# Optimization experiments

Hardware: AMD Instinct MI355X
Metric: run time of the kernel (lower is better)

Reference implementation:

```python
import jax, jax.numpy as jnp
import numpy as np

T, B, NIN = 256, 256, 512
NH, NEMB = 512, 256


def setup_inputs() -> dict:
    key = jax.random.key(0)
    ks = jax.random.split(key, 11)
    s = 0.02  # small init to keep tanh/sigmoid in active range
    return {
        "feats": jax.random.normal(ks[0], (T, B, NIN), jnp.float32),
        "h": jax.random.normal(ks[1], (B, NH), jnp.float32),
        "cur_embed": jax.random.normal(ks[2], (B, NEMB), jnp.float32),
        # i2h: Linear(nIn, nHidden, bias=False)
        "w_i2h": jax.random.normal(ks[3], (NH, NIN), jnp.float32) * s,
        # h2h: Linear(nHidden, nHidden) with bias
        "w_h2h": jax.random.normal(ks[4], (NH, NH), jnp.float32) * s,
        "b_h2h": jax.random.normal(ks[5], (NH,), jnp.float32) * s,
        # score: Linear(nHidden, 1, bias=False)
        "w_score": jax.random.normal(ks[6], (NH,), jnp.float32) * s,
        # GRUCell(nIn + num_embeddings, nHidden); gate order r, z, n
        "w_ih": jax.random.normal(ks[7], (3 * NH, NIN + NEMB), jnp.float32) * s,
        "w_hh": jax.random.normal(ks[8], (3 * NH, NH), jnp.float32) * s,
        "b_ih": jax.random.normal(ks[9], (3 * NH,), jnp.float32) * s,
        "b_hh": jax.random.normal(ks[10], (3 * NH,), jnp.float32) * s,
    }


def reference(feats, h, cur_embed, w_i2h, w_h2h, b_h2h, w_score,
              w_ih, w_hh, b_ih, b_hh):
    # MORAN branch, test=True (FractionalPickup is skipped at eval time).
    # feats: [T, B, nIn], h: [B, nHidden], cur_embed: [B, nEmb]
    feats_ = jnp.einsum('tbc,hc->tbh', feats, w_i2h)          # i2h, [T,B,H]
    h_ = h @ w_h2h.T + b_h2h                                   # h2h, [B,H]
    emit = jnp.einsum('tbh,h->tb', jnp.tanh(feats_ + h_[None]), w_score)
    alpha = jax.nn.softmax(emit, axis=0)                       # softmax over T
    context = jnp.einsum('tb,tbc->bc', alpha, feats)           # [B,nIn]
    x = jnp.concatenate([context, cur_embed], axis=1)          # [B,nIn+nEmb]
    # GRUCell
    gi = x @ w_ih.T + b_ih                                     # [B,3H]
    gh = h @ w_hh.T + b_hh                                     # [B,3H]
    gi_r, gi_z, gi_n = jnp.split(gi, 3, axis=1)
    gh_r, gh_z, gh_n = jnp.split(gh, 3, axis=1)
    r = jax.nn.sigmoid(gi_r + gh_r)
    z = jax.nn.sigmoid(gi_z + gh_z)
    n = jnp.tanh(gi_n + r * gh_n)
    nh = (1.0 - z) * n + z * h
    return nh, alpha
```

## Files before the change

kernel.cpp:

```cpp
#include <hip/hip_runtime.h>

typedef __bf16 bf16;
typedef __bf16 bf16x4 __attribute__((ext_vector_type(4)));
typedef __bf16 bf16x8 __attribute__((ext_vector_type(8)));
typedef float  f32x4  __attribute__((ext_vector_type(4)));

#define T_DIM 256
#define B_DIM 256
#define NIN   512
#define NH    512
#define NEMB  256
#define NX    768
#define NG    1536

__device__ __forceinline__ float fast_tanh(float x) {
    float e = __expf(2.0f * x);
    return 1.0f - 2.0f * __builtin_amdgcn_rcpf(e + 1.0f);
}
__device__ __forceinline__ float fast_sigmoid(float x) {
    return __builtin_amdgcn_rcpf(1.0f + __expf(-x));
}

__device__ __forceinline__ void gload_lds16(const bf16* g, bf16* l) {
    __builtin_amdgcn_global_load_lds(
        (const __attribute__((address_space(1))) void*)g,
        (__attribute__((address_space(3))) void*)l, 16, 0, 0);
}

__device__ __forceinline__ int swz(int rc) { return ((rc >> 1) & 3) << 3; }

__global__ __launch_bounds__(256) void cvt_weights(
    const float* __restrict__ a0, const float* __restrict__ a1,
    const float* __restrict__ a2, const float* __restrict__ a3,
    const float* __restrict__ a4,
    bf16* __restrict__ b0, bf16* __restrict__ b1, bf16* __restrict__ b2,
    bf16* __restrict__ b3, bf16* __restrict__ b4) {
    const int N0 = 65536, N1 = 131072, N2 = 425984, N3 = 622592, N4 = 655360;
    for (int i = blockIdx.x * 256 + threadIdx.x; i < N4; i += gridDim.x * 256) {
        const float* s; bf16* d; int j; bool img = false;
        if (i < N0)      { s = a0; d = b0; j = i; img = true; }
        else if (i < N1) { s = a1; d = b1; j = i - N0; }
        else if (i < N2) { s = a2; d = b2; j = i - N1; }
        else if (i < N3) { s = a3; d = b3; j = i - N2; }
        else             { s = a4; d = b4; j = i - N3; }
        float4 v = reinterpret_cast<const float4*>(s)[j];
        bf16x4 o = { (bf16)v.x, (bf16)v.y, (bf16)v.z, (bf16)v.w };
        if (img) {
            int e = j * 4, col = e >> 9, kc = e & 511, kk = kc >> 5, k = kc & 31;
            int off = kk * 16384 + col * 32 + (k ^ swz(col));
            *reinterpret_cast<bf16x4*>(d + off) = o;
        } else {
            reinterpret_cast<bf16x4*>(d)[j] = o;
        }
    }
}

__global__ __launch_bounds__(256) void gemm_bias(
    const bf16* __restrict__ A, const bf16* __restrict__ B,
    const float* __restrict__ bias, float* __restrict__ C,
    int M, int N, int K) {
    __shared__ bf16 At[64][40];
    __shared__ bf16 Bt[64][40];
    const int tid = threadIdx.x;
    const int m0 = blockIdx.y * 64, n0 = blockIdx.x * 64;
    const int wid = tid >> 6, lane = tid & 63, hi = lane >> 4, lo = lane & 15;
    const int srow = tid >> 2, sseg = tid & 3;
    f32x4 acc[4] = {};

    for (int kk = 0; kk < K; kk += 32) {
        bf16x8 av = *reinterpret_cast<const bf16x8*>(A + (size_t)(m0 + srow) * K + kk + sseg * 8);
        bf16x8 bv = *reinterpret_cast<const bf16x8*>(B + (size_t)(n0 + srow) * K + kk + sseg * 8);
        __syncthreads();
        *reinterpret_cast<bf16x8*>(&At[srow][sseg * 8]) = av;
        *reinterpret_cast<bf16x8*>(&Bt[srow][sseg * 8]) = bv;
        __syncthreads();
        bf16x8 a = *reinterpret_cast<const bf16x8*>(&At[wid * 16 + lo][hi * 8]);
#pragma unroll
        for (int nt = 0; nt < 4; ++nt) {
            bf16x8 b = *reinterpret_cast<const bf16x8*>(&Bt[nt * 16 + lo][hi * 8]);
            acc[nt] = __builtin_amdgcn_mfma_f32_16x16x32_bf16(a, b, acc[nt], 0, 0, 0);
        }
    }
#pragma unroll
    for (int nt = 0; nt < 4; ++nt) {
        int n = n0 + nt * 16 + lo;
        float bv = bias[n];
#pragma unroll
        for (int r = 0; r < 4; ++r) {
            int m = m0 + wid * 16 + hi * 4 + r;
            C[(size_t)m * N + n] = acc[nt][r] + bv;
        }
    }
}

__global__ __launch_bounds__(512, 4) void emit_kernel(
    const float* __restrict__ feats, const bf16* __restrict__ Wimg,
    const float* __restrict__ hbuf, const float* __restrict__ wscore,
    float* __restrict__ emit_out) {
    __shared__ bf16 Btile[2][16384];
    __shared__ bf16 Atile[2][2048];
    __shared__ float ew[512];
    const int tid = threadIdx.x;
    const int m0 = blockIdx.x * 64;
    const int wid = tid >> 6, lane = tid & 63, hi = lane >> 4, lo = lane & 15;

    const int arow = tid >> 3, akq = tid & 7;
    const int aoff = arow * 32 + ((akq * 4) ^ swz(arow));
    const float* asrc = feats + (size_t)(m0 + arow) * NIN + akq * 4;

#pragma unroll
    for (int r = 0; r < 4; ++r)
        gload_lds16(Wimg + r * 4096 + wid * 512 + lane * 8,
                    &Btile[0][r * 4096 + wid * 512]);
    {
        float4 fa = *reinterpret_cast<const float4*>(asrc);
        bf16x4 o = { (bf16)fa.x, (bf16)fa.y, (bf16)fa.z, (bf16)fa.w };
        *reinterpret_cast<bf16x4*>(&Atile[0][aoff]) = o;
    }
    __syncthreads();

    f32x4 acc[4][4] = {};
    float4 fa;
    for (int kk = 0; kk < 16; ++kk) {
        const int cur = kk & 1, nxt = cur ^ 1;
        if (kk < 15) {
            fa = *reinterpret_cast<const float4*>(asrc + (kk + 1) * 32);
#pragma unroll
            for (int r = 0; r < 4; ++r)
                gload_lds16(Wimg + (kk + 1) * 16384 + r * 4096 + wid * 512 + lane * 8,
                            &Btile[nxt][r * 4096 + wid * 512]);
        }

        bf16x8 a[4], b[4];
#pragma unroll
        for (int st = 0; st < 4; ++st) {
            int row = st * 16 + lo;
            a[st] = *reinterpret_cast<const bf16x8*>(
                &Atile[cur][row * 32 + ((hi * 8) ^ swz(row))]);
        }
#pragma unroll
        for (int nt = 0; nt < 4; ++nt) {
            int col = wid * 64 + nt * 16 + lo;
            b[nt] = *reinterpret_cast<const bf16x8*>(
                &Btile[cur][col * 32 + ((hi * 8) ^ swz(col))]);
        }
#pragma unroll
        for (int nt = 0; nt < 4; ++nt)
#pragma unroll
            for (int st = 0; st < 4; ++st)
                acc[nt][st] = __builtin_amdgcn_mfma_f32_16x16x32_bf16(a[st], b[nt], acc[nt][st], 0, 0, 0);

        if (kk < 15) {
            bf16x4 o = { (bf16)fa.x, (bf16)fa.y, (bf16)fa.z, (bf16)fa.w };
            *reinterpret_cast<bf16x4*>(&Atile[nxt][aoff]) = o;
        }
        __syncthreads();
    }

    float ep[4][4] = {};
    const int bbase = m0 & (B_DIM - 1);
    const int n0 = wid * 64;
#pragma unroll
    for (int nt = 0; nt < 4; ++nt) {
        int n = n0 + nt * 16 + lo;
        float wsn = wscore[n];
#pragma unroll
        for (int st = 0; st < 4; ++st) {
#pragma unroll
            for (int r = 0; r < 4; ++r) {
                int b = bbase + st * 16 + hi * 4 + r;
                float x = acc[nt][st][r] + hbuf[(size_t)b * NH + n];
                ep[st][r] += fast_tanh(x) * wsn;
            }
        }
    }
#pragma unroll
    for (int st = 0; st < 4; ++st)
#pragma unroll
        for (int r = 0; r < 4; ++r)
#pragma unroll
            for (int off = 1; off < 16; off <<= 1)
                ep[st][r] += __shfl_xor(ep[st][r], off, 64);

    if (lo == 0) {
#pragma unroll
        for (int st = 0; st < 4; ++st)
#pragma unroll
            for (int r = 0; r < 4; ++r)
                ew[wid * 64 + st * 16 + hi * 4 + r] = ep[st][r];
    }
    __syncthreads();
    if (tid < 64) {
        float s = 0.0f;
#pragma unroll
        for (int ww = 0; ww < 8; ++ww) s += ew[ww * 64 + tid];
        emit_out[m0 + tid] = s;
    }
}

__global__ __launch_bounds__(256) void softmax_t(
    const float* __restrict__ emit, float* __restrict__ alpha, float* __restrict__ out_alpha) {
    int b = blockIdx.x, t = threadIdx.x;
    int wv = t >> 6, ln = t & 63;
    float e = emit[(size_t)t * B_DIM + b];
    float m = e;
#pragma unroll
    for (int off = 32; off; off >>= 1) m = fmaxf(m, __shfl_xor(m, off, 64));
    __shared__ float red[4], red2[4];
    if (ln == 0) red[wv] = m;
    __syncthreads();
    m = fmaxf(fmaxf(red[0], red[1]), fmaxf(red[2], red[3]));
    float p = __expf(e - m);
    float s = p;
#pragma unroll
    for (int off = 32; off; off >>= 1) s += __shfl_xor(s, off, 64);
    if (ln == 0) red2[wv] = s;
    __syncthreads();
    float inv = __builtin_amdgcn_rcpf(red2[0] + red2[1] + red2[2] + red2[3]);
    float a = p * inv;
    alpha[(size_t)t * B_DIM + b] = a;
    out_alpha[(size_t)t * B_DIM + b] = a;
}

__global__ __launch_bounds__(256) void ctx_kernel(
    const float* __restrict__ feats, const float* __restrict__ alpha,
    const float* __restrict__ emb, bf16* __restrict__ x) {
    int b = blockIdx.x;
    __shared__ float al[T_DIM];
    __shared__ float red[4][512];
    int tid = threadIdx.x;
    al[tid] = alpha[(size_t)tid * B_DIM + b];
    __syncthreads();
    int c8 = tid & 63, tq = tid >> 6;
    float acc[8] = {};
    for (int t = tq * 64; t < tq * 64 + 64; ++t) {
        const float* src = feats + ((size_t)(t * B_DIM + b)) * NIN + c8 * 8;
        float4 v0 = *reinterpret_cast<const float4*>(src);
        float4 v1 = *reinterpret_cast<const float4*>(src + 4);
        float a = al[t];
        acc[0] += a * v0.x; acc[1] += a * v0.y; acc[2] += a * v0.z; acc[3] += a * v0.w;
        acc[4] += a * v1.x; acc[5] += a * v1.y; acc[6] += a * v1.z; acc[7] += a * v1.w;
    }
#pragma unroll
    for (int j = 0; j < 8; ++j) red[tq][c8 * 8 + j] = acc[j];
    __syncthreads();
#pragma unroll
    for (int k = 0; k < 2; ++k) {
        int c = tid * 2 + k;
        float s = red[0][c] + red[1][c] + red[2][c] + red[3][c];
        x[(size_t)b * NX + c] = (bf16)s;
    }
    x[(size_t)b * NX + NIN + tid] = (bf16)emb[(size_t)b * NEMB + tid];
}

__global__ __launch_bounds__(256) void gru_kernel(
    const float* __restrict__ gi, const float* __restrict__ gh,
    const float* __restrict__ h, float* __restrict__ out) {
    int idx = blockIdx.x * 256 + threadIdx.x;
    int b = idx >> 9, j = idx & 511;
    const float* gib = gi + (size_t)b * NG;
    const float* ghb = gh + (size_t)b * NG;
    float r = fast_sigmoid(gib[j] + ghb[j]);
    float z = fast_sigmoid(gib[NH + j] + ghb[NH + j]);
    float n = fast_tanh(gib[2 * NH + j] + r * ghb[2 * NH + j]);
    out[idx] = (1.0f - z) * n + z * h[idx];
}

extern "C" void kernel_launch(void* const* d_in, const int* in_sizes, int n_in,
                              void* d_out, int out_size, void* d_ws, size_t ws_size,
                              hipStream_t stream) {
    const float* feats = (const float*)d_in[0];
    const float* h     = (const float*)d_in[1];
    const float* emb   = (const float*)d_in[2];
    const float* w_i2h = (const float*)d_in[3];
    const float* w_h2h = (const float*)d_in[4];
    const float* b_h2h = (const float*)d_in[5];
    const float* w_sc  = (const float*)d_in[6];
    const float* w_ih  = (const float*)d_in[7];
    const float* w_hh  = (const float*)d_in[8];
    const float* b_ih  = (const float*)d_in[9];
    const float* b_hh  = (const float*)d_in[10];
    float* out = (float*)d_out;

    char* ws = (char*)d_ws;
    bf16*  Wimg    = (bf16*)(ws);
    bf16*  w_h2h_b = (bf16*)(ws + 524288);
    bf16*  w_ih_b  = (bf16*)(ws + 1048576);
    bf16*  w_hh_b  = (bf16*)(ws + 3407872);
    bf16*  h_b     = (bf16*)(ws + 4980736);
    bf16*  x_b     = (bf16*)(ws + 5242880);
    float* hbuf    = (float*)(ws + 5636096);
    float* emit    = (float*)(ws + 6160384);
    float* alpha   = (float*)(ws + 6422528);
    float* gi      = (float*)(ws + 6684672);
    float* gh      = (float*)(ws + 8257536);

    cvt_weights<<<1024, 256, 0, stream>>>(w_i2h, w_h2h, w_ih, w_hh, h,
                                          Wimg, w_h2h_b, w_ih_b, w_hh_b, h_b);

    gemm_bias<<<dim3(8, 4), 256, 0, stream>>>(h_b, w_h2h_b, b_h2h, hbuf, 256, NH, NH);

    emit_kernel<<<1024, 512, 0, stream>>>(feats, Wimg, hbuf, w_sc, emit);

    softmax_t<<<256, 256, 0, stream>>>(emit, alpha, out + 131072);

    ctx_kernel<<<256, 256, 0, stream>>>(feats, alpha, emb, x_b);

    gemm_bias<<<dim3(24, 4), 256, 0, stream>>>(x_b, w_ih_b, b_ih, gi, 256, NG, NX);
    gemm_bias<<<dim3(24, 4), 256, 0, stream>>>(h_b, w_hh_b, b_hh, gh, 256, NG, NH);

    gru_kernel<<<512, 256, 0, stream>>>(gi, gh, h, out);
}
```

Measured before the change: 122.6 us.

## Load attention weight fragments directly into registers with deeper prefetch in emit kernel

The emit GEMM no longer stages the bf16 image-projection weights through a double-buffered LDS tile via global_load_lds. Each lane now reads its B fragments straight from global memory into registers, three stages deep, and feats is prefetched three iterations ahead. The loop is fully unrolled with hand-placed waitcnt and barriers in place of __syncthreads. This cuts about 64KB of LDS and the LDS round trip for B, but raises register pressure, so launch bounds drop from 4 to 2 blocks per CU. It also relies on the pre-swizzled weight layout being readable with per-lane global loads.

```diff
diff --git a/kernel.cpp b/kernel.cpp
--- a/kernel.cpp
+++ b/kernel.cpp
@@ -19,12 +19,6 @@
 }
 __device__ __forceinline__ float fast_sigmoid(float x) {
     return __builtin_amdgcn_rcpf(1.0f + __expf(-x));
-}
-
-__device__ __forceinline__ void gload_lds16(const bf16* g, bf16* l) {
-    __builtin_amdgcn_global_load_lds(
-        (const __attribute__((address_space(1))) void*)g,
-        (__attribute__((address_space(3))) void*)l, 16, 0, 0);
 }
 
 __device__ __forceinline__ int swz(int rc) { return ((rc >> 1) & 3) << 3; }
@@ -93,11 +87,10 @@
     }
 }
 
-__global__ __launch_bounds__(512, 4) void emit_kernel(
+__global__ __launch_bounds__(512, 2) void emit_kernel(
     const float* __restrict__ feats, const bf16* __restrict__ Wimg,
     const float* __restrict__ hbuf, const float* __restrict__ wscore,
     float* __restrict__ emit_out) {
-    __shared__ bf16 Btile[2][16384];
     __shared__ bf16 Atile[2][2048];
     __shared__ float ew[512];
     const int tid = threadIdx.x;
@@ -108,53 +101,61 @@
     const int aoff = arow * 32 + ((akq * 4) ^ swz(arow));
     const float* asrc = feats + (size_t)(m0 + arow) * NIN + akq * 4;
 
-#pragma unroll
-    for (int r = 0; r < 4; ++r)
-        gload_lds16(Wimg + r * 4096 + wid * 512 + lane * 8,
-                    &Btile[0][r * 4096 + wid * 512]);
+    const int col0 = wid * 64 + lo;
+    const bf16* bsrc = Wimg + col0 * 32 + ((hi * 8) ^ swz(col0));
+
+    float4 fa[3];
+    bf16x8 bfr[3][4];
+
+    fa[0] = *reinterpret_cast<const float4*>(asrc);
+    fa[1] = *reinterpret_cast<const float4*>(asrc + 32);
+    fa[2] = *reinterpret_cast<const float4*>(asrc + 64);
+#pragma unroll
+    for (int s = 0; s < 2; ++s)
+#pragma unroll
+        for (int nt = 0; nt < 4; ++nt)
+            bfr[s][nt] = *reinterpret_cast<const bf16x8*>(bsrc + s * 16384 + nt * 512);
     {
-        float4 fa = *reinterpret_cast<const float4*>(asrc);
-        bf16x4 o = { (bf16)fa.x, (bf16)fa.y, (bf16)fa.z, (bf16)fa.w };
+        bf16x4 o = { (bf16)fa[0].x, (bf16)fa[0].y, (bf16)fa[0].z, (bf16)fa[0].w };
         *reinterpret_cast<bf16x4*>(&Atile[0][aoff]) = o;
     }
-    __syncthreads();
+    asm volatile("s_waitcnt lgkmcnt(0)" ::: "memory");
+    __builtin_amdgcn_s_barrier();
+    __builtin_amdgcn_sched_barrier(0);
 
     f32x4 acc[4][4] = {};
-    float4 fa;
+#pragma unroll
     for (int kk = 0; kk < 16; ++kk) {
-        const int cur = kk & 1, nxt = cur ^ 1;
-        if (kk < 15) {
-            fa = *reinterpret_cast<const float4*>(asrc + (kk + 1) * 32);
-#pragma unroll
-            for (int r = 0; r < 4; ++r)
-                gload_lds16(Wimg + (kk + 1) * 16384 + r * 4096 + wid * 512 + lane * 8,
-                            &Btile[nxt][r * 4096 + wid * 512]);
-        }
-
-        bf16x8 a[4], b[4];
+        if (kk + 3 < 16)
+            fa[kk % 3] = *reinterpret_cast<const float4*>(asrc + (kk + 3) * 32);
+        if (kk + 2 < 16) {
+#pragma unroll
+            for (int nt = 0; nt < 4; ++nt)
+                bfr[(kk + 2) % 3][nt] =
+                    *reinterpret_cast<const bf16x8*>(bsrc + (kk + 2) * 16384 + nt * 512);
+        }
+        bf16x8 a[4];
 #pragma unroll
         for (int st = 0; st < 4; ++st) {
             int row = st * 16 + lo;
             a[st] = *reinterpret_cast<const bf16x8*>(
-                &Atile[cur][row * 32 + ((hi * 8) ^ swz(row))]);
-        }
-#pragma unroll
-        for (int nt = 0; nt < 4; ++nt) {
-            int col = wid * 64 + nt * 16 + lo;
-            b[nt] = *reinterpret_cast<const bf16x8*>(
-                &Btile[cur][col * 32 + ((hi * 8) ^ swz(col))]);
+                &Atile[kk & 1][row * 32 + ((hi * 8) ^ swz(row))]);
         }
 #pragma unroll
         for (int nt = 0; nt < 4; ++nt)
 #pragma unroll
             for (int st = 0; st < 4; ++st)
-                acc[nt][st] = __builtin_amdgcn_mfma_f32_16x16x32_bf16(a[st], b[nt], acc[nt][st], 0, 0, 0);
-
-        if (kk < 15) {
-            bf16x4 o = { (bf16)fa.x, (bf16)fa.y, (bf16)fa.z, (bf16)fa.w };
-            *reinterpret_cast<bf16x4*>(&Atile[nxt][aoff]) = o;
-        }
-        __syncthreads();
+                acc[nt][st] = __builtin_amdgcn_mfma_f32_16x16x32_bf16(
+                    a[st], bfr[kk % 3][nt], acc[nt][st], 0, 0, 0);
+        if (kk + 1 < 16) {
+            float4 f = fa[(kk + 1) % 3];
+            bf16x4 o = { (bf16)f.x, (bf16)f.y, (bf16)f.z, (bf16)f.w };
+            *reinterpret_cast<bf16x4*>(&Atile[(kk + 1) & 1][aoff]) = o;
+            asm volatile("s_waitcnt lgkmcnt(0)" ::: "memory");
+            __builtin_amdgcn_sched_barrier(0);
+            __builtin_amdgcn_s_barrier();
+            __builtin_amdgcn_sched_barrier(0);
+        }
     }
 
     float ep[4][4] = {};
```

Result: slower. 128.3 us (+4.7%).

## Triple-buffer emit kernel B tiles with manual waitcnt and single barrier

Applied to the files above, without the earlier changes.

Converts the emit GEMM's weight tile staging from double to triple buffering with prefetch distance two. The per-iteration __syncthreads pair is replaced by explicit vmcnt/lgkmcnt waits and one s_barrier, and the loop is fully unrolled. This hides more global-load latency behind MFMA work, at the cost of more LDS (three 32KB B buffers), which drops the occupancy hint. The reduction scratch now reuses Atile, and the h-to-hidden GRU GEMM launch is moved earlier in the stream with no functional change.

```diff
diff --git a/kernel.cpp b/kernel.cpp
--- a/kernel.cpp
+++ b/kernel.cpp
@@ -93,13 +93,12 @@
     }
 }
 
-__global__ __launch_bounds__(512, 4) void emit_kernel(
+__global__ __launch_bounds__(512) void emit_kernel(
     const float* __restrict__ feats, const bf16* __restrict__ Wimg,
     const float* __restrict__ hbuf, const float* __restrict__ wscore,
     float* __restrict__ emit_out) {
-    __shared__ bf16 Btile[2][16384];
+    __shared__ bf16 Btile[3][16384];
     __shared__ bf16 Atile[2][2048];
-    __shared__ float ew[512];
     const int tid = threadIdx.x;
     const int m0 = blockIdx.x * 64;
     const int wid = tid >> 6, lane = tid & 63, hi = lane >> 4, lo = lane & 15;
@@ -108,27 +107,44 @@
     const int aoff = arow * 32 + ((akq * 4) ^ swz(arow));
     const float* asrc = feats + (size_t)(m0 + arow) * NIN + akq * 4;
 
+    float4 fav0 = *reinterpret_cast<const float4*>(asrc);
+    float4 fav1 = *reinterpret_cast<const float4*>(asrc + 32);
 #pragma unroll
     for (int r = 0; r < 4; ++r)
-        gload_lds16(Wimg + r * 4096 + wid * 512 + lane * 8,
+        gload_lds16(Wimg + 0 * 16384 + r * 4096 + wid * 512 + lane * 8,
                     &Btile[0][r * 4096 + wid * 512]);
+#pragma unroll
+    for (int r = 0; r < 4; ++r)
+        gload_lds16(Wimg + 1 * 16384 + r * 4096 + wid * 512 + lane * 8,
+                    &Btile[1][r * 4096 + wid * 512]);
     {
-        float4 fa = *reinterpret_cast<const float4*>(asrc);
-        bf16x4 o = { (bf16)fa.x, (bf16)fa.y, (bf16)fa.z, (bf16)fa.w };
+        bf16x4 o = { (bf16)fav0.x, (bf16)fav0.y, (bf16)fav0.z, (bf16)fav0.w };
         *reinterpret_cast<bf16x4*>(&Atile[0][aoff]) = o;
     }
-    __syncthreads();
+    asm volatile("s_waitcnt lgkmcnt(0)" ::: "memory");
+    __builtin_amdgcn_sched_barrier(0);
 
     f32x4 acc[4][4] = {};
-    float4 fa;
+
+#pragma unroll
     for (int kk = 0; kk < 16; ++kk) {
-        const int cur = kk & 1, nxt = cur ^ 1;
         if (kk < 15) {
-            fa = *reinterpret_cast<const float4*>(asrc + (kk + 1) * 32);
+            asm volatile("s_waitcnt vmcnt(5)" ::: "memory");
+        } else {
+            asm volatile("s_waitcnt vmcnt(0)" ::: "memory");
+        }
+        __builtin_amdgcn_s_barrier();
+        __builtin_amdgcn_sched_barrier(0);
+
+        if (kk < 14) {
+            if ((kk & 1) == 0)
+                fav0 = *reinterpret_cast<const float4*>(asrc + (kk + 2) * 32);
+            else
+                fav1 = *reinterpret_cast<const float4*>(asrc + (kk + 2) * 32);
 #pragma unroll
             for (int r = 0; r < 4; ++r)
-                gload_lds16(Wimg + (kk + 1) * 16384 + r * 4096 + wid * 512 + lane * 8,
-                            &Btile[nxt][r * 4096 + wid * 512]);
+                gload_lds16(Wimg + (kk + 2) * 16384 + r * 4096 + wid * 512 + lane * 8,
+                            &Btile[(kk + 2) % 3][r * 4096 + wid * 512]);
         }
 
         bf16x8 a[4], b[4];
@@ -136,25 +152,28 @@
         for (int st = 0; st < 4; ++st) {
             int row = st * 16 + lo;
             a[st] = *reinterpret_cast<const bf16x8*>(
-                &Atile[cur][row * 32 + ((hi * 8) ^ swz(row))]);
+                &Atile[kk & 1][row * 32 + ((hi * 8) ^ swz(row))]);
         }
 #pragma unroll
         for (int nt = 0; nt < 4; ++nt) {
             int col = wid * 64 + nt * 16 + lo;
             b[nt] = *reinterpret_cast<const bf16x8*>(
-                &Btile[cur][col * 32 + ((hi * 8) ^ swz(col))]);
+                &Btile[kk % 3][col * 32 + ((hi * 8) ^ swz(col))]);
         }
 #pragma unroll
         for (int nt = 0; nt < 4; ++nt)
 #pragma unroll
             for (int st = 0; st < 4; ++st)
-                acc[nt][st] = __builtin_amdgcn_mfma_f32_16x16x32_bf16(a[st], b[nt], acc[nt][st], 0, 0, 0);
+                acc[nt][st] = __builtin_amdgcn_mfma_f32_16x16x32_bf16(
+                    a[st], b[nt], acc[nt][st], 0, 0, 0);
 
         if (kk < 15) {
-            bf16x4 o = { (bf16)fa.x, (bf16)fa.y, (bf16)fa.z, (bf16)fa.w };
-            *reinterpret_cast<bf16x4*>(&Atile[nxt][aoff]) = o;
-        }
-        __syncthreads();
+            float4 f = ((kk + 1) & 1) ? fav1 : fav0;
+            bf16x4 o = { (bf16)f.x, (bf16)f.y, (bf16)f.z, (bf16)f.w };
+            *reinterpret_cast<bf16x4*>(&Atile[(kk + 1) & 1][aoff]) = o;
+            asm volatile("s_waitcnt lgkmcnt(0)" ::: "memory");
+            __builtin_amdgcn_sched_barrier(0);
+        }
     }
 
     float ep[4][4] = {};
@@ -182,6 +201,8 @@
             for (int off = 1; off < 16; off <<= 1)
                 ep[st][r] += __shfl_xor(ep[st][r], off, 64);
 
+    __syncthreads();
+    float* ew = reinterpret_cast<float*>(&Atile[0][0]);
     if (lo == 0) {
 #pragma unroll
         for (int st = 0; st < 4; ++st)
@@ -299,6 +320,7 @@
                                           Wimg, w_h2h_b, w_ih_b, w_hh_b, h_b);
 
     gemm_bias<<<dim3(8, 4), 256, 0, stream>>>(h_b, w_h2h_b, b_h2h, hbuf, 256, NH, NH);
+    gemm_bias<<<dim3(24, 4), 256, 0, stream>>>(h_b, w_hh_b, b_hh, gh, 256, NG, NH);
 
     emit_kernel<<<1024, 512, 0, stream>>>(feats, Wimg, hbuf, w_sc, emit);
 
@@ -307,7 +329,6 @@
     ctx_kernel<<<256, 256, 0, stream>>>(feats, alpha, emb, x_b);
 
     gemm_bias<<<dim3(24, 4), 256, 0, stream>>>(x_b, w_ih_b, b_ih, gi, 256, NG, NX);
-    gemm_bias<<<dim3(24, 4), 256, 0, stream>>>(h_b, w_hh_b, b_hh, gh, 256, NG, NH);
 
     gru_kernel<<<512, 256, 0, stream>>>(gi, gh, h, out);
 }
```

Result: slower. 141.0 us (+15.0%).

## Enlarge emit GEMM tile to 128 rows with 64-wide K stages

Applied to the files above, without the earlier changes.

The emit kernel now computes 128 rows per block instead of 64, with K stages of 64 and a single LDS buffer. The weight image layout and swizzle are changed to match (8-slot XOR on 16-byte chunks). Each block loads the full weight tile once per stage, so weight traffic per output row is halved and there are fewer barrier rounds. The cost is no double buffering (two syncs per stage), higher register and LDS use (occupancy hint lowered to 2), and half as many blocks. The gh GEMM is also moved earlier and the ctx loop gets an unroll hint.

```diff
diff --git a/kernel.cpp b/kernel.cpp
--- a/kernel.cpp
+++ b/kernel.cpp
@@ -12,6 +12,7 @@
 #define NEMB  256
 #define NX    768
 #define NG    1536
+#define MTOT  65536
 
 __device__ __forceinline__ float fast_tanh(float x) {
     float e = __expf(2.0f * x);
@@ -26,8 +27,6 @@
         (const __attribute__((address_space(1))) void*)g,
         (__attribute__((address_space(3))) void*)l, 16, 0, 0);
 }
-
-__device__ __forceinline__ int swz(int rc) { return ((rc >> 1) & 3) << 3; }
 
 __global__ __launch_bounds__(256) void cvt_weights(
     const float* __restrict__ a0, const float* __restrict__ a1,
@@ -46,9 +45,10 @@
         float4 v = reinterpret_cast<const float4*>(s)[j];
         bf16x4 o = { (bf16)v.x, (bf16)v.y, (bf16)v.z, (bf16)v.w };
         if (img) {
-            int e = j * 4, col = e >> 9, kc = e & 511, kk = kc >> 5, k = kc & 31;
-            int off = kk * 16384 + col * 32 + (k ^ swz(col));
-            *reinterpret_cast<bf16x4*>(d + off) = o;
+            int e = j * 4, col = e >> 9, K = e & 511;
+            int st = K >> 6, k = K & 63, chunk = k >> 3, within = k & 7;
+            int slot = chunk ^ (col & 7);
+            *reinterpret_cast<bf16x4*>(d + st * 32768 + col * 64 + slot * 8 + within) = o;
         } else {
             reinterpret_cast<bf16x4*>(d)[j] = o;
         }
@@ -93,89 +93,108 @@
     }
 }
 
-__global__ __launch_bounds__(512, 4) void emit_kernel(
+__global__ __launch_bounds__(512, 2) void emit_kernel(
     const float* __restrict__ feats, const bf16* __restrict__ Wimg,
     const float* __restrict__ hbuf, const float* __restrict__ wscore,
     float* __restrict__ emit_out) {
-    __shared__ bf16 Btile[2][16384];
-    __shared__ bf16 Atile[2][2048];
-    __shared__ float ew[512];
+    __shared__ bf16 Bt[512 * 64];
+    __shared__ bf16 At[128 * 64];
+    __shared__ float ew[8][128];
     const int tid = threadIdx.x;
-    const int m0 = blockIdx.x * 64;
+    const int m0 = blockIdx.x * 128;
     const int wid = tid >> 6, lane = tid & 63, hi = lane >> 4, lo = lane & 15;
 
-    const int arow = tid >> 3, akq = tid & 7;
-    const int aoff = arow * 32 + ((akq * 4) ^ swz(arow));
-    const float* asrc = feats + (size_t)(m0 + arow) * NIN + akq * 4;
-
-#pragma unroll
-    for (int r = 0; r < 4; ++r)
+    const int arow = tid >> 2, ac = tid & 3;
+    const float* asrc = feats + (size_t)(m0 + arow) * NIN + ac * 16;
+    bf16* aw0 = At + arow * 64 + (((2 * ac) ^ (arow & 7)) * 8);
+    bf16* aw1 = At + arow * 64 + (((2 * ac + 1) ^ (arow & 7)) * 8);
+
+    float4 va0, va1, va2, va3;
+    va0 = *reinterpret_cast<const float4*>(asrc);
+    va1 = *reinterpret_cast<const float4*>(asrc + 4);
+    va2 = *reinterpret_cast<const float4*>(asrc + 8);
+    va3 = *reinterpret_cast<const float4*>(asrc + 12);
+#pragma unroll
+    for (int r = 0; r < 8; ++r)
         gload_lds16(Wimg + r * 4096 + wid * 512 + lane * 8,
-                    &Btile[0][r * 4096 + wid * 512]);
+                    Bt + r * 4096 + wid * 512);
     {
-        float4 fa = *reinterpret_cast<const float4*>(asrc);
-        bf16x4 o = { (bf16)fa.x, (bf16)fa.y, (bf16)fa.z, (bf16)fa.w };
-        *reinterpret_cast<bf16x4*>(&Atile[0][aoff]) = o;
-    }
-    __syncthreads();
-
-    f32x4 acc[4][4] = {};
-    float4 fa;
-    for (int kk = 0; kk < 16; ++kk) {
-        const int cur = kk & 1, nxt = cur ^ 1;
-        if (kk < 15) {
-            fa = *reinterpret_cast<const float4*>(asrc + (kk + 1) * 32);
-#pragma unroll
-            for (int r = 0; r < 4; ++r)
-                gload_lds16(Wimg + (kk + 1) * 16384 + r * 4096 + wid * 512 + lane * 8,
-                            &Btile[nxt][r * 4096 + wid * 512]);
-        }
-
-        bf16x8 a[4], b[4];
-#pragma unroll
-        for (int st = 0; st < 4; ++st) {
-            int row = st * 16 + lo;
-            a[st] = *reinterpret_cast<const bf16x8*>(
-                &Atile[cur][row * 32 + ((hi * 8) ^ swz(row))]);
-        }
+        bf16x8 o0 = { (bf16)va0.x, (bf16)va0.y, (bf16)va0.z, (bf16)va0.w,
+                      (bf16)va1.x, (bf16)va1.y, (bf16)va1.z, (bf16)va1.w };
+        bf16x8 o1 = { (bf16)va2.x, (bf16)va2.y, (bf16)va2.z, (bf16)va2.w,
+                      (bf16)va3.x, (bf16)va3.y, (bf16)va3.z, (bf16)va3.w };
+        *reinterpret_cast<bf16x8*>(aw0) = o0;
+        *reinterpret_cast<bf16x8*>(aw1) = o1;
+    }
+    __syncthreads();
+
+    f32x4 acc[8][4] = {};
+    for (int s = 0; s < 8; ++s) {
+        if (s < 7) {
+            const float* an = asrc + (s + 1) * 64;
+            va0 = *reinterpret_cast<const float4*>(an);
+            va1 = *reinterpret_cast<const float4*>(an + 4);
+            va2 = *reinterpret_cast<const float4*>(an + 8);
+            va3 = *reinterpret_cast<const float4*>(an + 12);
+        }
+        bf16x8 b[4][2];
 #pragma unroll
         for (int nt = 0; nt < 4; ++nt) {
             int col = wid * 64 + nt * 16 + lo;
-            b[nt] = *reinterpret_cast<const bf16x8*>(
-                &Btile[cur][col * 32 + ((hi * 8) ^ swz(col))]);
-        }
-#pragma unroll
-        for (int nt = 0; nt < 4; ++nt)
-#pragma unroll
-            for (int st = 0; st < 4; ++st)
-                acc[nt][st] = __builtin_amdgcn_mfma_f32_16x16x32_bf16(a[st], b[nt], acc[nt][st], 0, 0, 0);
-
-        if (kk < 15) {
-            bf16x4 o = { (bf16)fa.x, (bf16)fa.y, (bf16)fa.z, (bf16)fa.w };
-            *reinterpret_cast<bf16x4*>(&Atile[nxt][aoff]) = o;
+#pragma unroll
+            for (int k2 = 0; k2 < 2; ++k2)
+                b[nt][k2] = *reinterpret_cast<const bf16x8*>(
+                    Bt + col * 64 + (((k2 * 4 + hi) ^ (col & 7)) * 8));
+        }
+#pragma unroll
+        for (int st = 0; st < 8; ++st) {
+            int row = st * 16 + lo;
+            bf16x8 a0 = *reinterpret_cast<const bf16x8*>(
+                At + row * 64 + ((hi ^ (row & 7)) * 8));
+            bf16x8 a1 = *reinterpret_cast<const bf16x8*>(
+                At + row * 64 + (((4 + hi) ^ (row & 7)) * 8));
+#pragma unroll
+            for (int nt = 0; nt < 4; ++nt) {
+                acc[st][nt] = __builtin_amdgcn_mfma_f32_16x16x32_bf16(a0, b[nt][0], acc[st][nt], 0, 0, 0);
+                acc[st][nt] = __builtin_amdgcn_mfma_f32_16x16x32_bf16(a1, b[nt][1], acc[st][nt], 0, 0, 0);
+            }
         }
         __syncthreads();
-    }
-
-    float ep[4][4] = {};
+        if (s < 7) {
+            bf16x8 o0 = { (bf16)va0.x, (bf16)va0.y, (bf16)va0.z, (bf16)va0.w,
+                          (bf16)va1.x, (bf16)va1.y, (bf16)va1.z, (bf16)va1.w };
+            bf16x8 o1 = { (bf16)va2.x, (bf16)va2.y, (bf16)va2.z, (bf16)va2.w,
+                          (bf16)va3.x, (bf16)va3.y, (bf16)va3.z, (bf16)va3.w };
+            *reinterpret_cast<bf16x8*>(aw0) = o0;
+            *reinterpret_cast<bf16x8*>(aw1) = o1;
+#pragma unroll
+            for (int r = 0; r < 8; ++r)
+                gload_lds16(Wimg + (s + 1) * 32768 + r * 4096 + wid * 512 + lane * 8,
+                            Bt + r * 4096 + wid * 512);
+            __syncthreads();
+        }
+    }
+
     const int bbase = m0 & (B_DIM - 1);
-    const int n0 = wid * 64;
-#pragma unroll
-    for (int nt = 0; nt < 4; ++nt) {
-        int n = n0 + nt * 16 + lo;
-        float wsn = wscore[n];
-#pragma unroll
-        for (int st = 0; st < 4; ++st) {
-#pragma unroll
-            for (int r = 0; r < 4; ++r) {
-                int b = bbase + st * 16 + hi * 4 + r;
-                float x = acc[nt][st][r] + hbuf[(size_t)b * NH + n];
-                ep[st][r] += fast_tanh(x) * wsn;
-            }
-        }
-    }
-#pragma unroll
-    for (int st = 0; st < 4; ++st)
+    float ws4[4];
+#pragma unroll
+    for (int nt = 0; nt < 4; ++nt) ws4[nt] = wscore[wid * 64 + nt * 16 + lo];
+    float ep[8][4];
+#pragma unroll
+    for (int st = 0; st < 8; ++st) {
+#pragma unroll
+        for (int r = 0; r < 4; ++r) {
+            int brow = bbase + st * 16 + hi * 4 + r;
+            const float* hp = hbuf + (size_t)brow * NH + wid * 64 + lo;
+            float e = 0.0f;
+#pragma unroll
+            for (int nt = 0; nt < 4; ++nt)
+                e += fast_tanh(acc[st][nt][r] + hp[nt * 16]) * ws4[nt];
+            ep[st][r] = e;
+        }
+    }
+#pragma unroll
+    for (int st = 0; st < 8; ++st)
 #pragma unroll
         for (int r = 0; r < 4; ++r)
 #pragma unroll
@@ -184,33 +203,35 @@
 
     if (lo == 0) {
 #pragma unroll
-        for (int st = 0; st < 4; ++st)
+        for (int st = 0; st < 8; ++st)
 #pragma unroll
             for (int r = 0; r < 4; ++r)
-                ew[wid * 64 + st * 16 + hi * 4 + r] = ep[st][r];
-    }
-    __syncthreads();
-    if (tid < 64) {
-        float s = 0.0f;
-#pragma unroll
-        for (int ww = 0; ww < 8; ++ww) s += ew[ww * 64 + tid];
-        emit_out[m0 + tid] = s;
+                ew[wid][st * 16 + hi * 4 + r] = ep[st][r];
+    }
+    __syncthreads();
+    if (tid < 128) {
+        float sacc = 0.0f;
+#pragma unroll
+        for (int ww = 0; ww < 8; ++ww) sacc += ew[ww][tid];
+        emit_out[m0 + tid] = sacc;
     }
 }
 
 __global__ __launch_bounds__(256) void softmax_t(
-    const float* __restrict__ emit, float* __restrict__ alpha, float* __restrict__ out_alpha) {
+    const float* __restrict__ emit, float* __restrict__ alpha,
+    float* __restrict__ out_alpha) {
     int b = blockIdx.x, t = threadIdx.x;
     int wv = t >> 6, ln = t & 63;
-    float e = emit[(size_t)t * B_DIM + b];
-    float m = e;
-#pragma unroll
-    for (int off = 32; off; off >>= 1) m = fmaxf(m, __shfl_xor(m, off, 64));
+    size_t m = (size_t)t * B_DIM + b;
+    float e = emit[m];
+    float mx = e;
+#pragma unroll
+    for (int off = 32; off; off >>= 1) mx = fmaxf(mx, __shfl_xor(mx, off, 64));
     __shared__ float red[4], red2[4];
-    if (ln == 0) red[wv] = m;
-    __syncthreads();
-    m = fmaxf(fmaxf(red[0], red[1]), fmaxf(red[2], red[3]));
-    float p = __expf(e - m);
+    if (ln == 0) red[wv] = mx;
+    __syncthreads();
+    mx = fmaxf(fmaxf(red[0], red[1]), fmaxf(red[2], red[3]));
+    float p = __expf(e - mx);
     float s = p;
 #pragma unroll
     for (int off = 32; off; off >>= 1) s += __shfl_xor(s, off, 64);
@@ -218,8 +239,8 @@
     __syncthreads();
     float inv = __builtin_amdgcn_rcpf(red2[0] + red2[1] + red2[2] + red2[3]);
     float a = p * inv;
-    alpha[(size_t)t * B_DIM + b] = a;
-    out_alpha[(size_t)t * B_DIM + b] = a;
+    alpha[m] = a;
+    out_alpha[m] = a;
 }
 
 __global__ __launch_bounds__(256) void ctx_kernel(
@@ -233,6 +254,7 @@
     __syncthreads();
     int c8 = tid & 63, tq = tid >> 6;
     float acc[8] = {};
+#pragma unroll 4
     for (int t = tq * 64; t < tq * 64 + 64; ++t) {
         const float* src = feats + ((size_t)(t * B_DIM + b)) * NIN + c8 * 8;
         float4 v0 = *reinterpret_cast<const float4*>(src);
@@ -299,15 +321,15 @@
                                           Wimg, w_h2h_b, w_ih_b, w_hh_b, h_b);
 
     gemm_bias<<<dim3(8, 4), 256, 0, stream>>>(h_b, w_h2h_b, b_h2h, hbuf, 256, NH, NH);
-
-    emit_kernel<<<1024, 512, 0, stream>>>(feats, Wimg, hbuf, w_sc, emit);
+    gemm_bias<<<dim3(24, 4), 256, 0, stream>>>(h_b, w_hh_b, b_hh, gh, 256, NG, NH);
+
+    emit_kernel<<<512, 512, 0, stream>>>(feats, Wimg, hbuf, w_sc, emit);
 
     softmax_t<<<256, 256, 0, stream>>>(emit, alpha, out + 131072);
 
     ctx_kernel<<<256, 256, 0, stream>>>(feats, alpha, emb, x_b);
 
     gemm_bias<<<dim3(24, 4), 256, 0, stream>>>(x_b, w_ih_b, b_ih, gi, 256, NG, NX);
-    gemm_bias<<<dim3(24, 4), 256, 0, stream>>>(h_b, w_hh_b, b_hh, gh, 256, NG, NH);
 
     gru_kernel<<<512, 256, 0, stream>>>(gi, gh, h, out);
 }
```

After: 123.1 us. About the same (+0.4%).
